# Performance work log

Measured on AMD Instinct MI355X. Metric: run time of the kernel, lower is better.

The kernel has to match this reference:

```python
import jax, jax.numpy as jnp
import numpy as np

B, LAT, NF, IMG, N_CALLS = 8, 512, 64, 128, 4
N_LAYERS = int(np.ceil(np.log2(IMG) - np.log2(16))) + 1  # 4 resolutions: 16,32,64,128
CF = 3  # SinSobel perception factor: identity + sobel_x + sobel_y
FIN, FH, FOUT = NF * CF, NF, NF * 2  # gated => 2*n_filter out of dyna block
P_SIZES = [FH * FIN, FH, FOUT * FH, FOUT, FOUT * FIN, FOUT]
P_OFFS = np.cumsum([0] + P_SIZES)
P_TOT = int(P_OFFS[-1])

_g1 = np.exp(-0.5 * np.array([-1.0, 0.0, 1.0]) ** 2)
_gk = np.outer(_g1, _g1); _gk = _gk / _gk.sum()
GAUSS_K = jnp.asarray(_gk, jnp.float32)
SOBEL_X = jnp.asarray(np.array([[-1, 0, 1], [-2, 0, 2], [-1, 0, 1]], np.float32) / 8.0)
SOBEL_Y = SOBEL_X.T


def _dwconv3(x, k):
    # depthwise 3x3 conv, 'same' padding; x: [B,C,H,W], k: [3,3]
    C = x.shape[1]
    kern = jnp.broadcast_to(k[None, None], (C, 1, 3, 3)).astype(x.dtype)
    return jax.lax.conv_general_dilated(
        x, kern, (1, 1), ((1, 1), (1, 1)),
        dimension_numbers=('NCHW', 'OIHW', 'NCHW'), feature_group_count=C)


def sin_sobel(x):
    # perception: [x, sobel_x(x), sobel_y(x)] -> 3*C channels
    return jnp.concatenate([x, _dwconv3(x, SOBEL_X), _dwconv3(x, SOBEL_Y)], axis=1)


def inst_norm(x, eps=1e-5):
    m = x.mean((2, 3), keepdims=True)
    v = x.var((2, 3), keepdims=True)
    return (x - m) * jax.lax.rsqrt(v + eps)


def up2_blur(x, gk):
    b, c, h, w = x.shape
    x = jax.image.resize(x, (b, c, 2 * h, 2 * w), 'bilinear')  # align_corners=False
    return _dwconv3(x, gk)


def dyna_block(x, lat, hyper_w, hyper_b):
    # hypernetwork generates per-sample 1x1-conv residual block weights
    p = lat @ hyper_w + hyper_b  # [B, P_TOT]
    w1 = p[:, P_OFFS[0]:P_OFFS[1]].reshape(-1, FH, FIN)
    b1 = p[:, P_OFFS[1]:P_OFFS[2]]
    w2 = p[:, P_OFFS[2]:P_OFFS[3]].reshape(-1, FOUT, FH)
    b2 = p[:, P_OFFS[3]:P_OFFS[4]]
    ws = p[:, P_OFFS[4]:P_OFFS[5]].reshape(-1, FOUT, FIN)
    bs = p[:, P_OFFS[5]:P_OFFS[6]]
    h = jax.nn.relu(jnp.einsum('bihw,boi->bohw', x, w1) + b1[:, :, None, None])
    y = jnp.einsum('bihw,boi->bohw', h, w2) + b2[:, :, None, None]
    s = jnp.einsum('bihw,boi->bohw', x, ws) + bs[:, :, None, None]
    return s + y


def setup_inputs() -> dict:
    key = jax.random.key(0)
    ks = jax.random.split(key, 8)
    return dict(
        lat=jax.random.normal(ks[0], (B, LAT), jnp.float32),
        ca_noise=jax.random.normal(ks[1], (B, NF, 16, 16), jnp.float32),
        seed=jax.random.normal(ks[2], (1, NF, 1, 1), jnp.float32),  # spatially constant seed
        leak_factor=jnp.asarray(0.1, jnp.float32),
        hyper_w=jax.random.normal(ks[3], (LAT, P_TOT), jnp.float32) * 0.02,
        hyper_b=jnp.zeros((P_TOT,), jnp.float32),
        res1_w=jax.random.normal(ks[4], (NF, NF), jnp.float32) / np.sqrt(NF).astype(np.float32),
        res1_b=jnp.zeros((NF,), jnp.float32),
        res2_w=jax.random.normal(ks[5], (NF, NF), jnp.float32) / np.sqrt(NF).astype(np.float32),
        res2_b=jnp.zeros((NF,), jnp.float32),
        outc_w=jax.random.normal(ks[6], (3, NF), jnp.float32) / np.sqrt(NF).astype(np.float32),
        outc_b=jnp.zeros((3,), jnp.float32),
    )


def reference(lat, ca_noise, seed, leak_factor, hyper_w, hyper_b,
              res1_w, res1_b, res2_w, res2_b, outc_w, outc_b):
    # seed init branch: constant seed -> instance_norm -> 0, plus blurred ca_noise
    out = inst_norm(jnp.broadcast_to(seed, (B, NF, 16, 16)))
    out = out + _dwconv3(ca_noise, GAUSS_K)  # in_ds (resize 16->16 is identity)
    lf = jnp.clip(leak_factor, 0.001, 1000.0)
    for c in range(N_LAYERS * N_CALLS):
        z = sin_sobel(out)
        z = inst_norm(z)
        z = dyna_block(z, lat, hyper_w, hyper_b)
        z, g = jnp.split(z, 2, axis=1)  # gated
        z = z * jax.nn.sigmoid(g)
        out = out + lf * z
        if c < N_LAYERS * N_CALLS - 1 and c % N_CALLS == N_CALLS - 1:
            out = up2_blur(out, GAUSS_K)
    # out_conv: resize to IMG is identity here; 1x1 residual block + 1x1 conv
    h = jax.nn.relu(jnp.einsum('bihw,oi->bohw', out, res1_w) + res1_b[None, :, None, None])
    r = jnp.einsum('bihw,oi->bohw', h, res2_w) + res2_b[None, :, None, None]
    y = jnp.einsum('bihw,oi->bohw', out + r, outc_w) + outc_b[None, :, None, None]
    out_raw = y
    return jnp.clip(y, -1.0, 1.0), out_raw
```

## Files before the change

kernel.cpp:

```cpp
#include <hip/hip_runtime.h>
#include <math.h>

#define B 8
#define LATD 512
#define PT 45376
#define FIN 192
#define FH 64
#define OW1 0
#define OB1 12288
#define OW2 12352
#define OB2 20544
#define OWS 20672
#define OBS 45248
#define KC 16

__device__ __forceinline__ float gk_at(int ky, int kx){
  const float a = 0.60653065971263342f;
  const float inv = 1.0f / ((1.0f + 2.0f*a) * (1.0f + 2.0f*a));
  float wy = (ky==1) ? 1.0f : a;
  float wx = (kx==1) ? 1.0f : a;
  return wy * wx * inv;
}

__global__ void k_hyper(const float* __restrict__ lat, const float* __restrict__ hw,
                        const float* __restrict__ hb, float* __restrict__ p){
  __shared__ float slat[B*LATD];
  for (int idx = threadIdx.x; idx < B*LATD; idx += 256) slat[idx] = lat[idx];
  __syncthreads();
  int j = blockIdx.x*256 + threadIdx.x;
  if (j >= PT) return;
  float acc[B];
#pragma unroll
  for (int b=0;b<B;++b) acc[b]=0.f;
  for (int k=0;k<LATD;++k){
    float w = hw[(size_t)k*PT + j];
#pragma unroll
    for (int b=0;b<B;++b) acc[b] = fmaf(slat[b*LATD+k], w, acc[b]);
  }
  float bias = hb[j];
#pragma unroll
  for (int b=0;b<B;++b) p[(size_t)b*PT + j] = acc[b] + bias;
}

__global__ void k_init(const float* __restrict__ noise, float* __restrict__ out){
  int bc = blockIdx.x;
  int t = threadIdx.x;
  int y = t >> 4, x = t & 15;
  const float* src = noise + (size_t)bc*256;
  float acc = 0.f;
#pragma unroll
  for (int ky=0;ky<3;++ky){
    int yy = y+ky-1; if (yy < 0 || yy > 15) continue;
#pragma unroll
    for (int kx=0;kx<3;++kx){
      int xx = x+kx-1; if (xx < 0 || xx > 15) continue;
      acc = fmaf(gk_at(ky,kx), src[yy*16+xx], acc);
    }
  }
  out[(size_t)bc*256 + t] = acc;
}

__global__ void __launch_bounds__(256) k_sobstat(const float* __restrict__ out, float* __restrict__ sob,
                    float* __restrict__ stats, int H, int lgH, int HW){
  int bc = blockIdx.x; int b = bc >> 6, c = bc & 63;
  int t = threadIdx.x;
  const float* src = out + ((size_t)(b*64+c))*(size_t)HW;
  float* dxp = sob + ((size_t)(b*128 + c))*(size_t)HW;
  float* dyp = sob + ((size_t)(b*128 + 64 + c))*(size_t)HW;
  float s0=0.f,q0=0.f,sx=0.f,qx=0.f,sy=0.f,qy=0.f;
  for (int px = t*4; px < HW; px += 1024){
    int y = px >> lgH, x = px & (H-1);
    float rm[6], rc[6], rp[6];
    float4 v = *(const float4*)(src + px);
    rc[1]=v.x; rc[2]=v.y; rc[3]=v.z; rc[4]=v.w;
    rc[0] = (x>0)     ? src[px-1] : 0.f;
    rc[5] = (x+4 < H) ? src[px+4] : 0.f;
    s0 += v.x+v.y+v.z+v.w;
    q0 += v.x*v.x+v.y*v.y+v.z*v.z+v.w*v.w;
    if (y > 0){
      const float* r = src + px - H;
      float4 u = *(const float4*)r;
      rm[1]=u.x; rm[2]=u.y; rm[3]=u.z; rm[4]=u.w;
      rm[0] = (x>0)     ? r[-1] : 0.f;
      rm[5] = (x+4 < H) ? r[4]  : 0.f;
    } else { rm[0]=rm[1]=rm[2]=rm[3]=rm[4]=rm[5]=0.f; }
    if (y+1 < H){
      const float* r = src + px + H;
      float4 u = *(const float4*)r;
      rp[1]=u.x; rp[2]=u.y; rp[3]=u.z; rp[4]=u.w;
      rp[0] = (x>0)     ? r[-1] : 0.f;
      rp[5] = (x+4 < H) ? r[4]  : 0.f;
    } else { rp[0]=rp[1]=rp[2]=rp[3]=rp[4]=rp[5]=0.f; }
    float dxv[4], dyv[4];
#pragma unroll
    for (int j=0;j<4;++j){
      dxv[j] = ((rm[j+2]-rm[j]) + 2.f*(rc[j+2]-rc[j]) + (rp[j+2]-rp[j])) * 0.125f;
      dyv[j] = ((rp[j] + 2.f*rp[j+1] + rp[j+2]) - (rm[j] + 2.f*rm[j+1] + rm[j+2])) * 0.125f;
      sx += dxv[j]; qx = fmaf(dxv[j],dxv[j],qx);
      sy += dyv[j]; qy = fmaf(dyv[j],dyv[j],qy);
    }
    float4 o1; o1.x=dxv[0]; o1.y=dxv[1]; o1.z=dxv[2]; o1.w=dxv[3];
    float4 o2; o2.x=dyv[0]; o2.y=dyv[1]; o2.z=dyv[2]; o2.w=dyv[3];
    *(float4*)(dxp + px) = o1;
    *(float4*)(dyp + px) = o2;
  }
  float vals[6] = {s0,q0,sx,qx,sy,qy};
  __shared__ float rbuf[6][4];
  int lane = t & 63, wid = t >> 6;
#pragma unroll
  for (int i=0;i<6;++i){
    float v = vals[i];
#pragma unroll
    for (int off=32; off; off>>=1) v += __shfl_down(v, off, 64);
    if (lane==0) rbuf[i][wid] = v;
  }
  __syncthreads();
  if (t < 3){
    float s = rbuf[t*2][0]+rbuf[t*2][1]+rbuf[t*2][2]+rbuf[t*2][3];
    float q = rbuf[t*2+1][0]+rbuf[t*2+1][1]+rbuf[t*2+1][2]+rbuf[t*2+1][3];
    float inv = 1.0f/(float)HW;
    float m = s*inv;
    float var = fmaxf(q*inv - m*m, 0.f);
    float r = 1.0f/sqrtf(var + 1e-5f);
    int ch = b*192 + c + t*64;
    stats[ch*2]   = -m*r;
    stats[ch*2+1] = r;
  }
}

__device__ __forceinline__ float4 ldx(const float* __restrict__ out, const float* __restrict__ sob,
                                      const float* __restrict__ stats,
                                      int b, int i, int off, int HW){
  const float* src = (i < 64) ? out + ((size_t)(b*64+i))*(size_t)HW
                              : sob + ((size_t)(b*128+(i-64)))*(size_t)HW;
  float4 v = *(const float4*)(src + off);
  float c = stats[(b*192+i)*2], r = stats[(b*192+i)*2+1];
  v.x = fmaf(v.x, r, c); v.y = fmaf(v.y, r, c);
  v.z = fmaf(v.z, r, c); v.w = fmaf(v.w, r, c);
  return v;
}

template<int PPT>
__global__ void __launch_bounds__(256, 3) k_dyna(float* __restrict__ out, const float* __restrict__ sob,
                       const float* __restrict__ stats, const float* __restrict__ p,
                       const float* __restrict__ lfp, int HW){
  constexpr int TPXT  = 16*PPT;
  constexpr int XST   = TPXT + 4;
  constexpr int XHALF = KC*XST;
  constexpr int W1OFF = 2*XHALF;
  constexpr int W1HALF= KC*68;
  constexpr int HSZ   = 64*XST;
  constexpr int ASZ   = (W1OFF + 2*W1HALF > HSZ) ? (W1OFF + 2*W1HALF) : HSZ;
  __shared__ float bufA[ASZ];
  __shared__ float bufB[2*KC*132];

  int b = blockIdx.y;
  int tx = threadIdx.x, ty = threadIdx.y;
  int tid = ty*16 + tx;
  int px0 = blockIdx.x*TPXT;
  const float* pw = p + (size_t)b*PT;

  float az[4][PPT], ag[4][PPT], ah[4][PPT];
#pragma unroll
  for (int k=0;k<4;++k)
#pragma unroll
    for (int j=0;j<PPT;++j){ az[k][j]=0.f; ag[k][j]=0.f; ah[k][j]=0.f; }

  const int wo0 = tid>>2, wk = tid&3, wo1 = 64 + wo0;

  float4 vx0, vx1, vz0, vz1, v10;

  auto loadX = [&](int ci){
    if constexpr (PPT==8){
      vx0 = ldx(out,sob,stats,b, ci*KC + (tid>>5),     px0 + (tid&31)*4, HW);
      vx1 = ldx(out,sob,stats,b, ci*KC + 8 + (tid>>5), px0 + (tid&31)*4, HW);
    } else {
      vx0 = ldx(out,sob,stats,b, ci*KC + (tid>>4),     px0 + (tid&15)*4, HW);
    }
  };
  auto loadW1z = [&](int ci){
    vz0 = *(const float4*)(pw + OWS + wo0*FIN + ci*KC + wk*4);
    vz1 = *(const float4*)(pw + OWS + wo1*FIN + ci*KC + wk*4);
    v10 = *(const float4*)(pw + OW1 + wo0*FIN + ci*KC + wk*4);
  };
  auto loadW2 = [&](int ci){
    vz0 = *(const float4*)(pw + OW2 + wo0*FH + ci*KC + wk*4);
    vz1 = *(const float4*)(pw + OW2 + wo1*FH + ci*KC + wk*4);
  };
  auto writeX = [&](int bf){
    if constexpr (PPT==8){
      *(float4*)(&bufA[bf*XHALF + (tid>>5)*XST     + (tid&31)*4]) = vx0;
      *(float4*)(&bufA[bf*XHALF + ((tid>>5)+8)*XST + (tid&31)*4]) = vx1;
    } else {
      *(float4*)(&bufA[bf*XHALF + (tid>>4)*XST     + (tid&15)*4]) = vx0;
    }
  };
  auto writeWz = [&](int bf){
    float* WZ = &bufB[bf*(KC*132)];
    WZ[(wk*4+0)*132+wo0]=vz0.x; WZ[(wk*4+1)*132+wo0]=vz0.y; WZ[(wk*4+2)*132+wo0]=vz0.z; WZ[(wk*4+3)*132+wo0]=vz0.w;
    WZ[(wk*4+0)*132+wo1]=vz1.x; WZ[(wk*4+1)*132+wo1]=vz1.y; WZ[(wk*4+2)*132+wo1]=vz1.z; WZ[(wk*4+3)*132+wo1]=vz1.w;
  };
  auto writeW1 = [&](int bf){
    float* W1 = &bufA[W1OFF + bf*W1HALF];
    W1[(wk*4+0)*68+wo0]=v10.x; W1[(wk*4+1)*68+wo0]=v10.y; W1[(wk*4+2)*68+wo0]=v10.z; W1[(wk*4+3)*68+wo0]=v10.w;
  };
  auto computeA = [&](int bf){
#pragma unroll 4
    for (int kk=0; kk<KC; ++kk){
      float4 xa  = *(const float4*)(&bufA[bf*XHALF + kk*XST + tx*4]);
      float4 wz4 = *(const float4*)(&bufB[bf*(KC*132) + kk*132 + ty*4]);
      float4 wg4 = *(const float4*)(&bufB[bf*(KC*132) + kk*132 + 64 + ty*4]);
      float4 w14 = *(const float4*)(&bufA[W1OFF + bf*W1HALF + kk*68 + ty*4]);
      float xv[PPT];
      xv[0]=xa.x; xv[1]=xa.y; xv[2]=xa.z; xv[3]=xa.w;
      if constexpr (PPT==8){
        float4 xb = *(const float4*)(&bufA[bf*XHALF + kk*XST + (tx+16)*4]);
        xv[4]=xb.x; xv[5]=xb.y; xv[6]=xb.z; xv[7]=xb.w;
      }
      float wzv[4]={wz4.x,wz4.y,wz4.z,wz4.w};
      float wgv[4]={wg4.x,wg4.y,wg4.z,wg4.w};
      float w1v[4]={w14.x,w14.y,w14.z,w14.w};
#pragma unroll
      for (int k=0;k<4;++k)
#pragma unroll
        for (int j=0;j<PPT;++j){
          az[k][j] = fmaf(wzv[k], xv[j], az[k][j]);
          ag[k][j] = fmaf(wgv[k], xv[j], ag[k][j]);
          ah[k][j] = fmaf(w1v[k], xv[j], ah[k][j]);
        }
    }
  };
  auto computeC = [&](int ci, int bf){
#pragma unroll 4
    for (int kk=0; kk<KC; ++kk){
      float4 xa  = *(const float4*)(&bufA[(ci*KC+kk)*XST + tx*4]);
      float4 wz4 = *(const float4*)(&bufB[bf*(KC*132) + kk*132 + ty*4]);
      float4 wg4 = *(const float4*)(&bufB[bf*(KC*132) + kk*132 + 64 + ty*4]);
      float xv[PPT];
      xv[0]=xa.x; xv[1]=xa.y; xv[2]=xa.z; xv[3]=xa.w;
      if constexpr (PPT==8){
        float4 xb = *(const float4*)(&bufA[(ci*KC+kk)*XST + (tx+16)*4]);
        xv[4]=xb.x; xv[5]=xb.y; xv[6]=xb.z; xv[7]=xb.w;
      }
      float wzv[4]={wz4.x,wz4.y,wz4.z,wz4.w};
      float wgv[4]={wg4.x,wg4.y,wg4.z,wg4.w};
#pragma unroll
      for (int k=0;k<4;++k)
#pragma unroll
        for (int j=0;j<PPT;++j){
          az[k][j] = fmaf(wzv[k], xv[j], az[k][j]);
          ag[k][j] = fmaf(wgv[k], xv[j], ag[k][j]);
        }
    }
  };

  loadX(0); loadW1z(0);
  writeX(0); writeWz(0); writeW1(0);
  loadX(1); loadW1z(1);
  __syncthreads();
  for (int ci=0; ci<12; ++ci){
    int cur = ci & 1;
    if (ci < 11){ writeX(cur^1); writeWz(cur^1); writeW1(cur^1); }
    if (ci < 10){ loadX(ci+2); loadW1z(ci+2); }
    else if (ci == 10){ loadW2(0); }
    computeA(cur);
    __syncthreads();
  }

#pragma unroll
  for (int k=0;k<4;++k){
    float b1 = pw[OB1 + ty*4 + k];
#pragma unroll
    for (int h=0; h<PPT/4; ++h){
      float4 r;
      r.x = fmaxf(ah[k][h*4+0]+b1, 0.f);
      r.y = fmaxf(ah[k][h*4+1]+b1, 0.f);
      r.z = fmaxf(ah[k][h*4+2]+b1, 0.f);
      r.w = fmaxf(ah[k][h*4+3]+b1, 0.f);
      *(float4*)(&bufA[(ty*4+k)*XST + (tx+h*16)*4]) = r;
    }
  }
  writeWz(0);
  loadW2(1);
  __syncthreads();

  for (int ci=0; ci<4; ++ci){
    int cur = ci & 1;
    if (ci < 3) writeWz(cur^1);
    if (ci < 2) loadW2(ci+2);
    computeC(ci, cur);
    __syncthreads();
  }

  float lf = fminf(fmaxf(lfp[0], 0.001f), 1000.f);
#pragma unroll
  for (int k=0;k<4;++k){
    int o = ty*4 + k;
    float bz = pw[OB2 + o]      + pw[OBS + o];
    float bg = pw[OB2 + o + 64] + pw[OBS + o + 64];
    float* op = out + ((size_t)(b*64+o))*(size_t)HW + px0;
#pragma unroll
    for (int h=0; h<PPT/4; ++h){
      float4 ov = *(const float4*)(op + (tx + h*16)*4);
      float r[4];
#pragma unroll
      for (int j=0;j<4;++j){
        float z = az[k][h*4+j] + bz;
        float g = ag[k][h*4+j] + bg;
        r[j] = lf * z / (1.f + expf(-g));
      }
      ov.x += r[0]; ov.y += r[1]; ov.z += r[2]; ov.w += r[3];
      *(float4*)(op + (tx + h*16)*4) = ov;
    }
  }
}

__global__ void k_upsample(const float* __restrict__ src, float* __restrict__ dst, int H, int lgH){
  int Hn = 2*H;
  int HWn = Hn*Hn;
  int bc = blockIdx.y;
  int o4 = (blockIdx.x*256 + threadIdx.x)*4;
  const float* s = src + (size_t)bc*(size_t)(H*H);
  int oy = o4 >> (lgH+1), ox0 = o4 & (Hn-1);
  int m = ox0 >> 1;
  int xm1 = (m-1 < 0)   ? 0   : m-1;
  int xp1 = (m+1 > H-1) ? H-1 : m+1;
  int xp2 = (m+2 > H-1) ? H-1 : m+2;
  float u[3][6];
#pragma unroll
  for (int ky=0; ky<3; ++ky){
    int yy = oy + ky - 1;
    if (yy < 0 || yy >= Hn){
#pragma unroll
      for (int j=0;j<6;++j) u[ky][j] = 0.f;
      continue;
    }
    int iy = yy >> 1, ry = yy & 1;
    int y0 = ry ? iy : iy-1;
    int y1 = ry ? iy+1 : iy;
    float wy0 = ry ? 0.75f : 0.25f;
    float wy1 = 1.f - wy0;
    y0 = y0 < 0 ? 0 : y0;
    y1 = y1 > H-1 ? H-1 : y1;
    const float* r0 = s + y0*H;
    const float* r1 = s + y1*H;
    float sv0 = wy0*r0[xm1] + wy1*r1[xm1];
    float sv1 = wy0*r0[m]   + wy1*r1[m];
    float sv2 = wy0*r0[xp1] + wy1*r1[xp1];
    float sv3 = wy0*r0[xp2] + wy1*r1[xp2];
    u[ky][0] = 0.75f*sv0 + 0.25f*sv1;
    u[ky][1] = 0.25f*sv0 + 0.75f*sv1;
    u[ky][2] = 0.75f*sv1 + 0.25f*sv2;
    u[ky][3] = 0.25f*sv1 + 0.75f*sv2;
    u[ky][4] = 0.75f*sv2 + 0.25f*sv3;
    u[ky][5] = 0.25f*sv2 + 0.75f*sv3;
    if (ox0 == 0)       u[ky][0] = 0.f;
    if (ox0 + 4 == Hn)  u[ky][5] = 0.f;
  }
  float res[4];
#pragma unroll
  for (int jo=0; jo<4; ++jo){
    float a = 0.f;
#pragma unroll
    for (int ky=0; ky<3; ++ky){
      a = fmaf(gk_at(ky,0), u[ky][jo],   a);
      a = fmaf(gk_at(ky,1), u[ky][jo+1], a);
      a = fmaf(gk_at(ky,2), u[ky][jo+2], a);
    }
    res[jo] = a;
  }
  float4 o; o.x=res[0]; o.y=res[1]; o.z=res[2]; o.w=res[3];
  *(float4*)(dst + (size_t)bc*(size_t)HWn + o4) = o;
}

__global__ void __launch_bounds__(256) k_final(const float* __restrict__ t,
    const float* __restrict__ r1w, const float* __restrict__ r1b,
    const float* __restrict__ r2w, const float* __restrict__ r2b,
    const float* __restrict__ ocw, const float* __restrict__ ocb,
    float* __restrict__ dout, int HW){
  __shared__ float Ts[64][132];
  __shared__ float Hs[64][132];
  __shared__ float Wb[64][68];
  int b = blockIdx.y;
  int tx = threadIdx.x, ty = threadIdx.y;
  int tid = ty*16 + tx;
  int px0 = blockIdx.x*128;

#pragma unroll
  for (int it=0; it<8; ++it){
    int idx = it*256 + tid;
    int ch = idx>>5, c4 = idx&31;
    *(float4*)(&Ts[ch][c4*4]) = *(const float4*)(t + ((size_t)(b*64+ch))*(size_t)HW + px0 + c4*4);
  }
#pragma unroll
  for (int it=0; it<4; ++it){
    int idx = it*256 + tid;
    int o = idx>>4, k4 = idx&15;
    float4 w = *(const float4*)(r1w + o*64 + k4*4);
    Wb[k4*4+0][o]=w.x; Wb[k4*4+1][o]=w.y; Wb[k4*4+2][o]=w.z; Wb[k4*4+3][o]=w.w;
  }
  __syncthreads();

  float acc[4][8];
#pragma unroll
  for (int k=0;k<4;++k)
#pragma unroll
    for (int j=0;j<8;++j) acc[k][j]=0.f;
#pragma unroll 4
  for (int kk=0; kk<64; ++kk){
    float4 xa = *(const float4*)(&Ts[kk][tx*4]);
    float4 xb = *(const float4*)(&Ts[kk][(tx+16)*4]);
    float4 w4 = *(const float4*)(&Wb[kk][ty*4]);
    float xv[8]={xa.x,xa.y,xa.z,xa.w,xb.x,xb.y,xb.z,xb.w};
    float wv[4]={w4.x,w4.y,w4.z,w4.w};
#pragma unroll
    for (int k=0;k<4;++k)
#pragma unroll
      for (int j=0;j<8;++j) acc[k][j] = fmaf(wv[k], xv[j], acc[k][j]);
  }
  __syncthreads();

#pragma unroll
  for (int k=0;k<4;++k){
    float bs = r1b[ty*4+k];
#pragma unroll
    for (int h=0; h<2; ++h){
      float4 r;
      r.x = fmaxf(acc[k][h*4+0]+bs, 0.f);
      r.y = fmaxf(acc[k][h*4+1]+bs, 0.f);
      r.z = fmaxf(acc[k][h*4+2]+bs, 0.f);
      r.w = fmaxf(acc[k][h*4+3]+bs, 0.f);
      *(float4*)(&Hs[ty*4+k][(tx+h*16)*4]) = r;
    }
  }
#pragma unroll
  for (int it=0; it<4; ++it){
    int idx = it*256 + tid;
    int o = idx>>4, k4 = idx&15;
    float4 w = *(const float4*)(r2w + o*64 + k4*4);
    Wb[k4*4+0][o]=w.x; Wb[k4*4+1][o]=w.y; Wb[k4*4+2][o]=w.z; Wb[k4*4+3][o]=w.w;
  }
  __syncthreads();

#pragma unroll
  for (int k=0;k<4;++k)
#pragma unroll
    for (int j=0;j<8;++j) acc[k][j]=0.f;
#pragma unroll 4
  for (int kk=0; kk<64; ++kk){
    float4 xa = *(const float4*)(&Hs[kk][tx*4]);
    float4 xb = *(const float4*)(&Hs[kk][(tx+16)*4]);
    float4 w4 = *(const float4*)(&Wb[kk][ty*4]);
    float xv[8]={xa.x,xa.y,xa.z,xa.w,xb.x,xb.y,xb.z,xb.w};
    float wv[4]={w4.x,w4.y,w4.z,w4.w};
#pragma unroll
    for (int k=0;k<4;++k)
#pragma unroll
      for (int j=0;j<8;++j) acc[k][j] = fmaf(wv[k], xv[j], acc[k][j]);
  }
#pragma unroll
  for (int k=0;k<4;++k){
    int o = ty*4 + k;
    float bs = r2b[o];
#pragma unroll
    for (int h=0; h<2; ++h){
      float4 tv = *(const float4*)(&Ts[o][(tx+h*16)*4]);
      tv.x += acc[k][h*4+0]+bs; tv.y += acc[k][h*4+1]+bs;
      tv.z += acc[k][h*4+2]+bs; tv.w += acc[k][h*4+3]+bs;
      *(float4*)(&Ts[o][(tx+h*16)*4]) = tv;
    }
  }
  __syncthreads();
  if (tid < 192){
    int c = tid>>6, kk = tid&63;
    Wb[kk][c] = ocw[c*64+kk];
  }
  __syncthreads();

  if (tid < 128){
    float a0=0.f, a1=0.f, a2=0.f;
#pragma unroll 4
    for (int kk=0; kk<64; ++kk){
      float x = Ts[kk][tid];
      a0 = fmaf(x, Wb[kk][0], a0);
      a1 = fmaf(x, Wb[kk][1], a1);
      a2 = fmaf(x, Wb[kk][2], a2);
    }
    size_t rawoff = (size_t)B*3*(size_t)HW;
    float y[3] = {a0+ocb[0], a1+ocb[1], a2+ocb[2]};
    int px = px0 + tid;
#pragma unroll
    for (int c=0;c<3;++c){
      size_t base = ((size_t)(b*3+c))*(size_t)HW + px;
      dout[base] = fminf(fmaxf(y[c],-1.f),1.f);
      dout[rawoff + base] = y[c];
    }
  }
}

extern "C" void kernel_launch(void* const* d_in, const int* in_sizes, int n_in,
                              void* d_out, int out_size, void* d_ws, size_t ws_size,
                              hipStream_t stream) {
  const float* lat = (const float*)d_in[0];
  const float* ca  = (const float*)d_in[1];
  const float* lfp = (const float*)d_in[3];
  const float* hw  = (const float*)d_in[4];
  const float* hb  = (const float*)d_in[5];
  const float* r1w = (const float*)d_in[6];
  const float* r1b = (const float*)d_in[7];
  const float* r2w = (const float*)d_in[8];
  const float* r2b = (const float*)d_in[9];
  const float* ocw = (const float*)d_in[10];
  const float* ocb = (const float*)d_in[11];
  float* dout = (float*)d_out;

  float* ws   = (float*)d_ws;
  float* p    = ws;
  float* outA = p    + (size_t)B*PT;
  float* outB = outA + (size_t)B*64*16384;
  float* sob  = outB + (size_t)B*64*16384;
  float* stats= sob  + (size_t)B*128*16384;

  k_hyper<<<dim3((PT+255)/256), dim3(256), 0, stream>>>(lat, hw, hb, p);
  k_init<<<dim3(B*64), dim3(256), 0, stream>>>(ca, outA);

  float* cur = outA;
  float* oth = outB;
  int H = 16, lgH = 4;
  for (int c = 0; c < 16; ++c){
    int HW = H*H;
    k_sobstat<<<dim3(B*64), dim3(256), 0, stream>>>(cur, sob, stats, H, lgH, HW);
    if (H >= 128)
      k_dyna<8><<<dim3(HW/128, B), dim3(16,16), 0, stream>>>(cur, sob, stats, p, lfp, HW);
    else
      k_dyna<4><<<dim3(HW/64,  B), dim3(16,16), 0, stream>>>(cur, sob, stats, p, lfp, HW);
    if (c < 15 && (c & 3) == 3){
      k_upsample<<<dim3((HW*4)/1024, B*64), dim3(256), 0, stream>>>(cur, oth, H, lgH);
      float* tmp = cur; cur = oth; oth = tmp;
      H *= 2; lgH += 1;
    }
  }
  int HW = H*H;
  k_final<<<dim3(HW/128, B), dim3(16,16), 0, stream>>>(cur, r1w, r1b, r2w, r2b, ocw, ocb, dout, HW);
}
```

Measured before the change: 1.350 ms.

## Use 16-pixel-per-thread dyna tiles at 128x128 with chunked hidden staging

At the 128x128 resolution the dyna kernel now handles 256 pixels per block (16 per thread) instead of 128, doubling reuse of each staged weight across pixels and halving the number of weight reloads per pixel. The hidden activations no longer fit in shared memory, so the second GEMM stages them in four 16-row chunks, each written by one quarter of the threads, with an extra sync per chunk and no double buffering of W2. The change raises register pressure (occupancy hint reduced to 2), which risks spills and lower latency hiding. It also folds the load/write/compute paths into generic loops over G float4 groups.

```diff
diff --git a/kernel.cpp b/kernel.cpp
--- a/kernel.cpp
+++ b/kernel.cpp
@@ -141,16 +141,18 @@
 }
 
 template<int PPT>
-__global__ void __launch_bounds__(256, 3) k_dyna(float* __restrict__ out, const float* __restrict__ sob,
+__global__ void __launch_bounds__(256, (PPT==16)?2:3) k_dyna(float* __restrict__ out, const float* __restrict__ sob,
                        const float* __restrict__ stats, const float* __restrict__ p,
                        const float* __restrict__ lfp, int HW){
+  constexpr int G     = PPT/4;
   constexpr int TPXT  = 16*PPT;
   constexpr int XST   = TPXT + 4;
   constexpr int XHALF = KC*XST;
   constexpr int W1OFF = 2*XHALF;
   constexpr int W1HALF= KC*68;
-  constexpr int HSZ   = 64*XST;
-  constexpr int ASZ   = (W1OFF + 2*W1HALF > HSZ) ? (W1OFF + 2*W1HALF) : HSZ;
+  constexpr int WEND  = W1OFF + 2*W1HALF;
+  constexpr int HSZ   = (PPT==16) ? 0 : 64*XST;
+  constexpr int ASZ   = (WEND > HSZ) ? WEND : HSZ;
   __shared__ float bufA[ASZ];
   __shared__ float bufB[2*KC*132];
 
@@ -168,14 +170,13 @@
 
   const int wo0 = tid>>2, wk = tid&3, wo1 = 64 + wo0;
 
-  float4 vx0, vx1, vz0, vz1, v10;
+  float4 vx[G], vz0, vz1, v10;
 
   auto loadX = [&](int ci){
-    if constexpr (PPT==8){
-      vx0 = ldx(out,sob,stats,b, ci*KC + (tid>>5),     px0 + (tid&31)*4, HW);
-      vx1 = ldx(out,sob,stats,b, ci*KC + 8 + (tid>>5), px0 + (tid&31)*4, HW);
-    } else {
-      vx0 = ldx(out,sob,stats,b, ci*KC + (tid>>4),     px0 + (tid&15)*4, HW);
+#pragma unroll
+    for (int g=0; g<G; ++g){
+      int idx = g*256 + tid;
+      vx[g] = ldx(out,sob,stats,b, ci*KC + idx/(4*PPT), px0 + (idx&(4*PPT-1))*4, HW);
     }
   };
   auto loadW1z = [&](int ci){
@@ -188,11 +189,10 @@
     vz1 = *(const float4*)(pw + OW2 + wo1*FH + ci*KC + wk*4);
   };
   auto writeX = [&](int bf){
-    if constexpr (PPT==8){
-      *(float4*)(&bufA[bf*XHALF + (tid>>5)*XST     + (tid&31)*4]) = vx0;
-      *(float4*)(&bufA[bf*XHALF + ((tid>>5)+8)*XST + (tid&31)*4]) = vx1;
-    } else {
-      *(float4*)(&bufA[bf*XHALF + (tid>>4)*XST     + (tid&15)*4]) = vx0;
+#pragma unroll
+    for (int g=0; g<G; ++g){
+      int idx = g*256 + tid;
+      *(float4*)(&bufA[bf*XHALF + (idx/(4*PPT))*XST + (idx&(4*PPT-1))*4]) = vx[g];
     }
   };
   auto writeWz = [&](int bf){
@@ -204,53 +204,36 @@
     float* W1 = &bufA[W1OFF + bf*W1HALF];
     W1[(wk*4+0)*68+wo0]=v10.x; W1[(wk*4+1)*68+wo0]=v10.y; W1[(wk*4+2)*68+wo0]=v10.z; W1[(wk*4+3)*68+wo0]=v10.w;
   };
+
+  auto bodyA = [&](int kk, int bf){
+    float xv[PPT];
+#pragma unroll
+    for (int g=0; g<G; ++g){
+      float4 xa = *(const float4*)(&bufA[bf*XHALF + kk*XST + (tx+g*16)*4]);
+      xv[g*4+0]=xa.x; xv[g*4+1]=xa.y; xv[g*4+2]=xa.z; xv[g*4+3]=xa.w;
+    }
+    float4 wz4 = *(const float4*)(&bufB[bf*(KC*132) + kk*132 + ty*4]);
+    float4 wg4 = *(const float4*)(&bufB[bf*(KC*132) + kk*132 + 64 + ty*4]);
+    float4 w14 = *(const float4*)(&bufA[W1OFF + bf*W1HALF + kk*68 + ty*4]);
+    float wzv[4]={wz4.x,wz4.y,wz4.z,wz4.w};
+    float wgv[4]={wg4.x,wg4.y,wg4.z,wg4.w};
+    float w1v[4]={w14.x,w14.y,w14.z,w14.w};
+#pragma unroll
+    for (int k=0;k<4;++k)
+#pragma unroll
+      for (int j=0;j<PPT;++j){
+        az[k][j] = fmaf(wzv[k], xv[j], az[k][j]);
+        ag[k][j] = fmaf(wgv[k], xv[j], ag[k][j]);
+        ah[k][j] = fmaf(w1v[k], xv[j], ah[k][j]);
+      }
+  };
   auto computeA = [&](int bf){
+    if constexpr (PPT==16){
+#pragma unroll 2
+      for (int kk=0; kk<KC; ++kk) bodyA(kk, bf);
+    } else {
 #pragma unroll 4
-    for (int kk=0; kk<KC; ++kk){
-      float4 xa  = *(const float4*)(&bufA[bf*XHALF + kk*XST + tx*4]);
-      float4 wz4 = *(const float4*)(&bufB[bf*(KC*132) + kk*132 + ty*4]);
-      float4 wg4 = *(const float4*)(&bufB[bf*(KC*132) + kk*132 + 64 + ty*4]);
-      float4 w14 = *(const float4*)(&bufA[W1OFF + bf*W1HALF + kk*68 + ty*4]);
-      float xv[PPT];
-      xv[0]=xa.x; xv[1]=xa.y; xv[2]=xa.z; xv[3]=xa.w;
-      if constexpr (PPT==8){
-        float4 xb = *(const float4*)(&bufA[bf*XHALF + kk*XST + (tx+16)*4]);
-        xv[4]=xb.x; xv[5]=xb.y; xv[6]=xb.z; xv[7]=xb.w;
-      }
-      float wzv[4]={wz4.x,wz4.y,wz4.z,wz4.w};
-      float wgv[4]={wg4.x,wg4.y,wg4.z,wg4.w};
-      float w1v[4]={w14.x,w14.y,w14.z,w14.w};
-#pragma unroll
-      for (int k=0;k<4;++k)
-#pragma unroll
-        for (int j=0;j<PPT;++j){
-          az[k][j] = fmaf(wzv[k], xv[j], az[k][j]);
-          ag[k][j] = fmaf(wgv[k], xv[j], ag[k][j]);
-          ah[k][j] = fmaf(w1v[k], xv[j], ah[k][j]);
-        }
-    }
-  };
-  auto computeC = [&](int ci, int bf){
-#pragma unroll 4
-    for (int kk=0; kk<KC; ++kk){
-      float4 xa  = *(const float4*)(&bufA[(ci*KC+kk)*XST + tx*4]);
-      float4 wz4 = *(const float4*)(&bufB[bf*(KC*132) + kk*132 + ty*4]);
-      float4 wg4 = *(const float4*)(&bufB[bf*(KC*132) + kk*132 + 64 + ty*4]);
-      float xv[PPT];
-      xv[0]=xa.x; xv[1]=xa.y; xv[2]=xa.z; xv[3]=xa.w;
-      if constexpr (PPT==8){
-        float4 xb = *(const float4*)(&bufA[(ci*KC+kk)*XST + (tx+16)*4]);
-        xv[4]=xb.x; xv[5]=xb.y; xv[6]=xb.z; xv[7]=xb.w;
-      }
-      float wzv[4]={wz4.x,wz4.y,wz4.z,wz4.w};
-      float wgv[4]={wg4.x,wg4.y,wg4.z,wg4.w};
-#pragma unroll
-      for (int k=0;k<4;++k)
-#pragma unroll
-        for (int j=0;j<PPT;++j){
-          az[k][j] = fmaf(wzv[k], xv[j], az[k][j]);
-          ag[k][j] = fmaf(wgv[k], xv[j], ag[k][j]);
-        }
+      for (int kk=0; kk<KC; ++kk) bodyA(kk, bf);
     }
   };
 
@@ -267,29 +250,93 @@
     __syncthreads();
   }
 
-#pragma unroll
-  for (int k=0;k<4;++k){
-    float b1 = pw[OB1 + ty*4 + k];
-#pragma unroll
-    for (int h=0; h<PPT/4; ++h){
-      float4 r;
-      r.x = fmaxf(ah[k][h*4+0]+b1, 0.f);
-      r.y = fmaxf(ah[k][h*4+1]+b1, 0.f);
-      r.z = fmaxf(ah[k][h*4+2]+b1, 0.f);
-      r.w = fmaxf(ah[k][h*4+3]+b1, 0.f);
-      *(float4*)(&bufA[(ty*4+k)*XST + (tx+h*16)*4]) = r;
-    }
-  }
-  writeWz(0);
-  loadW2(1);
-  __syncthreads();
-
-  for (int ci=0; ci<4; ++ci){
-    int cur = ci & 1;
-    if (ci < 3) writeWz(cur^1);
-    if (ci < 2) loadW2(ci+2);
-    computeC(ci, cur);
+  if constexpr (PPT==16){
+    for (int ci=0; ci<4; ++ci){
+      if (ci > 0) __syncthreads();
+      if ((ty>>2) == ci){
+        int lr = (ty&3)*4;
+#pragma unroll
+        for (int k=0;k<4;++k){
+          float b1 = pw[OB1 + ty*4 + k];
+#pragma unroll
+          for (int h=0; h<G; ++h){
+            float4 r;
+            r.x = fmaxf(ah[k][h*4+0]+b1, 0.f);
+            r.y = fmaxf(ah[k][h*4+1]+b1, 0.f);
+            r.z = fmaxf(ah[k][h*4+2]+b1, 0.f);
+            r.w = fmaxf(ah[k][h*4+3]+b1, 0.f);
+            *(float4*)(&bufA[(lr+k)*XST + (tx+h*16)*4]) = r;
+          }
+        }
+      }
+      writeWz(0);
+      if (ci < 3) loadW2(ci+1);
+      __syncthreads();
+#pragma unroll 2
+      for (int kk=0; kk<KC; ++kk){
+        float xv[PPT];
+#pragma unroll
+        for (int g=0; g<G; ++g){
+          float4 xa = *(const float4*)(&bufA[kk*XST + (tx+g*16)*4]);
+          xv[g*4+0]=xa.x; xv[g*4+1]=xa.y; xv[g*4+2]=xa.z; xv[g*4+3]=xa.w;
+        }
+        float4 wz4 = *(const float4*)(&bufB[kk*132 + ty*4]);
+        float4 wg4 = *(const float4*)(&bufB[kk*132 + 64 + ty*4]);
+        float wzv[4]={wz4.x,wz4.y,wz4.z,wz4.w};
+        float wgv[4]={wg4.x,wg4.y,wg4.z,wg4.w};
+#pragma unroll
+        for (int k=0;k<4;++k)
+#pragma unroll
+          for (int j=0;j<PPT;++j){
+            az[k][j] = fmaf(wzv[k], xv[j], az[k][j]);
+            ag[k][j] = fmaf(wgv[k], xv[j], ag[k][j]);
+          }
+      }
+    }
+  } else {
+#pragma unroll
+    for (int k=0;k<4;++k){
+      float b1 = pw[OB1 + ty*4 + k];
+#pragma unroll
+      for (int h=0; h<G; ++h){
+        float4 r;
+        r.x = fmaxf(ah[k][h*4+0]+b1, 0.f);
+        r.y = fmaxf(ah[k][h*4+1]+b1, 0.f);
+        r.z = fmaxf(ah[k][h*4+2]+b1, 0.f);
+        r.w = fmaxf(ah[k][h*4+3]+b1, 0.f);
+        *(float4*)(&bufA[(ty*4+k)*XST + (tx+h*16)*4]) = r;
+      }
+    }
+    writeWz(0);
+    loadW2(1);
     __syncthreads();
+
+    for (int ci=0; ci<4; ++ci){
+      int cur = ci & 1;
+      if (ci < 3) writeWz(cur^1);
+      if (ci < 2) loadW2(ci+2);
+#pragma unroll 4
+      for (int kk=0; kk<KC; ++kk){
+        float xv[PPT];
+#pragma unroll
+        for (int g=0; g<G; ++g){
+          float4 xa = *(const float4*)(&bufA[(ci*KC+kk)*XST + (tx+g*16)*4]);
+          xv[g*4+0]=xa.x; xv[g*4+1]=xa.y; xv[g*4+2]=xa.z; xv[g*4+3]=xa.w;
+        }
+        float4 wz4 = *(const float4*)(&bufB[cur*(KC*132) + kk*132 + ty*4]);
+        float4 wg4 = *(const float4*)(&bufB[cur*(KC*132) + kk*132 + 64 + ty*4]);
+        float wzv[4]={wz4.x,wz4.y,wz4.z,wz4.w};
+        float wgv[4]={wg4.x,wg4.y,wg4.z,wg4.w};
+#pragma unroll
+        for (int k=0;k<4;++k)
+#pragma unroll
+          for (int j=0;j<PPT;++j){
+            az[k][j] = fmaf(wzv[k], xv[j], az[k][j]);
+            ag[k][j] = fmaf(wgv[k], xv[j], ag[k][j]);
+          }
+      }
+      __syncthreads();
+    }
   }
 
   float lf = fminf(fmaxf(lfp[0], 0.001f), 1000.f);
@@ -300,7 +347,7 @@
     float bg = pw[OB2 + o + 64] + pw[OBS + o + 64];
     float* op = out + ((size_t)(b*64+o))*(size_t)HW + px0;
 #pragma unroll
-    for (int h=0; h<PPT/4; ++h){
+    for (int h=0; h<G; ++h){
       float4 ov = *(const float4*)(op + (tx + h*16)*4);
       float r[4];
 #pragma unroll
@@ -531,7 +578,7 @@
     int HW = H*H;
     k_sobstat<<<dim3(B*64), dim3(256), 0, stream>>>(cur, sob, stats, H, lgH, HW);
     if (H >= 128)
-      k_dyna<8><<<dim3(HW/128, B), dim3(16,16), 0, stream>>>(cur, sob, stats, p, lfp, HW);
+      k_dyna<16><<<dim3(HW/256, B), dim3(16,16), 0, stream>>>(cur, sob, stats, p, lfp, HW);
     else
       k_dyna<4><<<dim3(HW/64,  B), dim3(16,16), 0, stream>>>(cur, sob, stats, p, lfp, HW);
     if (c < 15 && (c & 3) == 3){
```

Measured after the change: 1.368 ms. No clear change (+1.3%).
